# Performance work log

Hardware: AMD Instinct MI355X
Metric: run time of the kernel (lower is better)

The kernel has to match this reference:

```python
import jax, jax.numpy as jnp
import numpy as np

B, L, D, H = 4, 1024, 1024, 16
DK = D // H


def setup_inputs() -> dict:
    key = jax.random.key(0)
    ks = jax.random.split(key, 5)
    s = 1.0 / np.sqrt(D)  # roughly nn.Linear init scale
    return {
        "x": jax.random.normal(ks[0], (B, L, D), dtype=jnp.float32),
        "Wq": jax.random.normal(ks[1], (D, D), dtype=jnp.float32) * s,
        "bq": jnp.zeros((D,), dtype=jnp.float32),
        "Wk": jax.random.normal(ks[2], (D, D), dtype=jnp.float32) * s,
        "bk": jnp.zeros((D,), dtype=jnp.float32),
        "Wv": jax.random.normal(ks[3], (D, D), dtype=jnp.float32) * s,
        "bv": jnp.zeros((D,), dtype=jnp.float32),
        "Wo": jax.random.normal(ks[4], (D, D), dtype=jnp.float32) * s,
        "bo": jnp.zeros((D,), dtype=jnp.float32),
    }


def reference(x, Wq, bq, Wk, bk, Wv, bv, Wo, bo):
    b, l, d = x.shape
    # torch Linear: y = x @ W.T + b
    q = (x @ Wq.T + bq).reshape(b, l, H, DK).transpose(0, 2, 1, 3)  # [B,H,L,DK]
    k = (x @ Wk.T + bk).reshape(b, l, H, DK).transpose(0, 2, 1, 3)
    v = (x @ Wv.T + bv).reshape(b, l, H, DK).transpose(0, 2, 1, 3)
    scores = jnp.einsum("bhqd,bhkd->bhqk", q, k) / jnp.sqrt(jnp.float32(DK))
    attn = jax.nn.softmax(scores, axis=-1)  # dropout p=0 -> identity
    head_out = jnp.einsum("bhqk,bhkd->bhqd", attn, v)  # [B,H,L,DK]
    merged = head_out.transpose(0, 2, 1, 3).reshape(b, l, d)  # [B,L,D]
    out = merged @ Wo.T + bo
    # DeCov loss over head outputs
    U = merged.reshape(b * l, d)
    U = U - U.mean(axis=0, keepdims=True)
    C = (U.T @ U) / jnp.float32(b * l)
    decov = 0.5 * (jnp.sum(C * C) - jnp.sum(jnp.diag(C) ** 2))
    return (out, decov)
```

## Files before the change

### kernel.cpp

```cpp
#include <hip/hip_runtime.h>
#include <cstdint>
#include <cstddef>

typedef short v4s __attribute__((ext_vector_type(4)));
typedef short v8s __attribute__((ext_vector_type(8)));
typedef float v4f __attribute__((ext_vector_type(4)));

__device__ __forceinline__ short f2bf(float f) {
    union { float f; unsigned u; } x; x.f = f;
    unsigned r = (x.u + 0x7FFFu + ((x.u >> 16) & 1u)) >> 16;
    return (short)(unsigned short)r;
}
__device__ __forceinline__ float bf2f(short h) {
    union { unsigned u; float f; } x; x.u = ((unsigned)(unsigned short)h) << 16;
    return x.f;
}

__device__ __forceinline__ void gld16(const void* g, void* l) {
    __builtin_amdgcn_global_load_lds((const __attribute__((address_space(1))) void*)g,
                                     (__attribute__((address_space(3))) void*)l, 16, 0, 0);
}

__global__ __launch_bounds__(256) void cvt_bf16(
    const float* __restrict__ x, const float* __restrict__ wq, const float* __restrict__ wk,
    const float* __restrict__ wv, const float* __restrict__ wo,
    short* __restrict__ xb, short* __restrict__ wqb, short* __restrict__ wkb,
    short* __restrict__ wvb, short* __restrict__ wob, float* __restrict__ colsum,
    float* __restrict__ dtot, int* __restrict__ dcnt)
{
    int bid = blockIdx.x;
    const float* src; short* dst; size_t base;
    if (bid < 4096)      { src = x;  dst = xb;  base = (size_t)bid * 1024; }
    else if (bid < 5120) { src = wq; dst = wqb; base = (size_t)(bid - 4096) * 1024; }
    else if (bid < 6144) { src = wk; dst = wkb; base = (size_t)(bid - 5120) * 1024; }
    else if (bid < 7168) { src = wv; dst = wvb; base = (size_t)(bid - 6144) * 1024; }
    else                 { src = wo; dst = wob; base = (size_t)(bid - 7168) * 1024; }
    size_t idx = base + (size_t)threadIdx.x * 4;
    v4f v = *(const v4f*)(src + idx);
    v4s o;
    o[0] = f2bf(v[0]); o[1] = f2bf(v[1]); o[2] = f2bf(v[2]); o[3] = f2bf(v[3]);
    *(v4s*)(dst + idx) = o;
    if (bid == 0) {
        v4f z = {0.f, 0.f, 0.f, 0.f};
        *(v4f*)(colsum + (size_t)threadIdx.x * 4) = z;
        if (threadIdx.x == 0) { *dtot = 0.f; *dcnt = 0; }
    }
}

__global__ __launch_bounds__(256) void gemm_qkv(
    const short* __restrict__ xb,
    const short* __restrict__ wq, const short* __restrict__ wk, const short* __restrict__ wv,
    const float* __restrict__ bq, const float* __restrict__ bk, const float* __restrict__ bv,
    short* __restrict__ qo, short* __restrict__ ko, short* __restrict__ vto)
{
    __shared__ __align__(16) short At[128 * 32];
    __shared__ __align__(16) short Bt[128 * 32];
    const int K = 1024;
    const int mode = blockIdx.z;
    const short* W = (mode == 0) ? wq : (mode == 1) ? wk : wv;
    const float* bias = (mode == 0) ? bq : (mode == 1) ? bk : bv;
    const int m0 = blockIdx.y * 128, n0 = blockIdx.x * 128;
    const int tid = threadIdx.x, wave = tid >> 6, lane = tid & 63;
    const int quad = lane >> 4, ll = lane & 15;
    const int wr = wave >> 1, wc = wave & 1;
    const v4f zero4 = {0.f, 0.f, 0.f, 0.f};
    v4f acc[4][4];
    for (int i = 0; i < 4; ++i) for (int j = 0; j < 4; ++j) acc[i][j] = zero4;

    for (int k0 = 0; k0 < K; k0 += 32) {
        __syncthreads();
#pragma unroll
        for (int c = 0; c < 2; ++c) {
            int chb = (wave * 2 + c) * 64;
            int ch = chb + lane;
            int row = ch >> 2, col8 = (ch & 3) * 8;
            gld16(xb + (size_t)(m0 + row) * K + k0 + col8, &At[chb * 8]);
            gld16(W  + (size_t)(n0 + row) * K + k0 + col8, &Bt[chb * 8]);
        }
        __syncthreads();
        v8s af[4], bfr[4];
#pragma unroll
        for (int i = 0; i < 4; ++i) af[i]  = *(const v8s*)&At[(wr * 64 + i * 16 + ll) * 32 + quad * 8];
#pragma unroll
        for (int j = 0; j < 4; ++j) bfr[j] = *(const v8s*)&Bt[(wc * 64 + j * 16 + ll) * 32 + quad * 8];
#pragma unroll
        for (int i = 0; i < 4; ++i)
#pragma unroll
            for (int j = 0; j < 4; ++j)
                acc[i][j] = __builtin_amdgcn_mfma_f32_16x16x32_bf16(af[i], bfr[j], acc[i][j], 0, 0, 0);
    }

    const float scale = (mode == 0) ? 0.125f : 1.0f;
#pragma unroll
    for (int j = 0; j < 4; ++j) {
        int n = n0 + wc * 64 + j * 16 + ll;
        float bb = bias[n];
        int hh = n >> 6, dk = n & 63;
#pragma unroll
        for (int i = 0; i < 4; ++i) {
            int mbase = m0 + wr * 64 + i * 16 + quad * 4;
#pragma unroll
            for (int r = 0; r < 4; ++r) {
                int m = mbase + r;
                int b = m >> 10, li = m & 1023;
                short h = f2bf((acc[i][j][r] + bb) * scale);
                if (mode == 0)
                    qo[(((size_t)(b * 16 + hh) * 1024 + li) << 6) + dk] = h;
                else if (mode == 1)
                    ko[(((size_t)(b * 16 + hh) * 1024 + li) << 6) + dk] = h;
                else
                    vto[(((size_t)(b * 16 + hh) * 64 + dk) << 10) + li] = h;
            }
        }
    }
}

__global__ __launch_bounds__(256) void attn_flash(
    const short* __restrict__ qb, const short* __restrict__ kb, const short* __restrict__ vtb,
    float* __restrict__ merged, short* __restrict__ mergedh, float* __restrict__ colsum)
{
    __shared__ __align__(16) short Kt[64 * 64];
    __shared__ __align__(16) short Vt[64 * 64];
    __shared__ __align__(16) short Pt[4 * 32 * 68];
    const int bh = blockIdx.y, qt = blockIdx.x;
    const int tid = threadIdx.x, wave = tid >> 6, lane = tid & 63;
    const int quad = lane >> 4, ll = lane & 15;
    const short* qp = qb  + (size_t)bh * 1024 * 64;
    const short* kp = kb  + (size_t)bh * 1024 * 64;
    const short* vp = vtb + (size_t)bh * 64 * 1024;

    v8s qa[2][2];
#pragma unroll
    for (int mi = 0; mi < 2; ++mi) {
        int qrow = qt * 128 + wave * 32 + mi * 16 + ll;
        qa[mi][0] = *(const v8s*)(qp + (size_t)qrow * 64 + quad * 8);
        qa[mi][1] = *(const v8s*)(qp + (size_t)qrow * 64 + 32 + quad * 8);
    }

    const v4f zero4 = {0.f, 0.f, 0.f, 0.f};
    v4f oacc[2][4];
    for (int mi = 0; mi < 2; ++mi) for (int nt = 0; nt < 4; ++nt) oacc[mi][nt] = zero4;
    float lsum[2][4];
    for (int mi = 0; mi < 2; ++mi) for (int r = 0; r < 4; ++r) lsum[mi][r] = 0.f;
    short* pw = &Pt[wave * 32 * 68];

    for (int jt = 0; jt < 16; ++jt) {
        __syncthreads();
#pragma unroll
        for (int c = 0; c < 2; ++c) {
            int chb = (wave * 2 + c) * 64;
            int ch = chb + lane;
            int row = ch >> 3;
            int gi = ((ch & 7) ^ (row & 7)) * 8;
            gld16(kp + (size_t)(jt * 64 + row) * 64 + gi, &Kt[chb * 8]);
            gld16(vp + (size_t)row * 1024 + jt * 64 + gi, &Vt[chb * 8]);
        }
        __syncthreads();

        v4f sacc[2][4];
#pragma unroll
        for (int nt = 0; nt < 4; ++nt) {
            int n = nt * 16 + ll;
            int g0 = (quad ^ (n & 7)) * 8;
            int g1 = ((4 + quad) ^ (n & 7)) * 8;
            v8s b0 = *(const v8s*)&Kt[n * 64 + g0];
            v8s b1 = *(const v8s*)&Kt[n * 64 + g1];
#pragma unroll
            for (int mi = 0; mi < 2; ++mi) {
                v4f s = zero4;
                s = __builtin_amdgcn_mfma_f32_16x16x32_bf16(qa[mi][0], b0, s, 0, 0, 0);
                s = __builtin_amdgcn_mfma_f32_16x16x32_bf16(qa[mi][1], b1, s, 0, 0, 0);
                sacc[mi][nt] = s;
            }
        }
#pragma unroll
        for (int mi = 0; mi < 2; ++mi)
#pragma unroll
            for (int nt = 0; nt < 4; ++nt)
#pragma unroll
                for (int r = 0; r < 4; ++r) {
                    float e = __expf(sacc[mi][nt][r]);
                    lsum[mi][r] += e;
                    pw[(mi * 16 + quad * 4 + r) * 68 + nt * 16 + ll] = f2bf(e);
                }
        v8s pa[2][2];
#pragma unroll
        for (int mi = 0; mi < 2; ++mi) {
            v4s p00 = *(const v4s*)&pw[(mi * 16 + ll) * 68 + quad * 8];
            v4s p01 = *(const v4s*)&pw[(mi * 16 + ll) * 68 + quad * 8 + 4];
            v4s p10 = *(const v4s*)&pw[(mi * 16 + ll) * 68 + 32 + quad * 8];
            v4s p11 = *(const v4s*)&pw[(mi * 16 + ll) * 68 + 32 + quad * 8 + 4];
            pa[mi][0] = __builtin_shufflevector(p00, p01, 0, 1, 2, 3, 4, 5, 6, 7);
            pa[mi][1] = __builtin_shufflevector(p10, p11, 0, 1, 2, 3, 4, 5, 6, 7);
        }
#pragma unroll
        for (int nt = 0; nt < 4; ++nt) {
            int n = nt * 16 + ll;
            int g0 = (quad ^ (n & 7)) * 8;
            int g1 = ((4 + quad) ^ (n & 7)) * 8;
            v8s v0 = *(const v8s*)&Vt[n * 64 + g0];
            v8s v1 = *(const v8s*)&Vt[n * 64 + g1];
#pragma unroll
            for (int mi = 0; mi < 2; ++mi) {
                oacc[mi][nt] = __builtin_amdgcn_mfma_f32_16x16x32_bf16(pa[mi][0], v0, oacc[mi][nt], 0, 0, 0);
                oacc[mi][nt] = __builtin_amdgcn_mfma_f32_16x16x32_bf16(pa[mi][1], v1, oacc[mi][nt], 0, 0, 0);
            }
        }
    }

    const int b = bh >> 4, h = bh & 15;
    float csum[4] = {0.f, 0.f, 0.f, 0.f};
#pragma unroll
    for (int mi = 0; mi < 2; ++mi) {
        float linv[4];
#pragma unroll
        for (int r = 0; r < 4; ++r) {
            float s = lsum[mi][r];
            s += __shfl_xor(s, 1); s += __shfl_xor(s, 2);
            s += __shfl_xor(s, 4); s += __shfl_xor(s, 8);
            linv[r] = 1.0f / s;
        }
#pragma unroll
        for (int r = 0; r < 4; ++r) {
            int li = qt * 128 + wave * 32 + mi * 16 + quad * 4 + r;
            size_t rowoff = ((size_t)(b * 1024 + li)) * 1024 + h * 64;
#pragma unroll
            for (int nt = 0; nt < 4; ++nt) {
                int d = nt * 16 + ll;
                float v = oacc[mi][nt][r] * linv[r];
                merged[rowoff + d] = v;
                mergedh[rowoff + d] = f2bf(v);
                csum[nt] += v;
            }
        }
    }
#pragma unroll
    for (int nt = 0; nt < 4; ++nt) {
        csum[nt] += __shfl_xor(csum[nt], 16);
        csum[nt] += __shfl_xor(csum[nt], 32);
    }
    if (quad == 0) {
#pragma unroll
        for (int nt = 0; nt < 4; ++nt)
            atomicAdd(&colsum[h * 64 + nt * 16 + ll], csum[nt]);
    }
}

__global__ __launch_bounds__(256) void post_attn(
    const short* __restrict__ A, const short* __restrict__ W, const float* __restrict__ bias,
    float* __restrict__ out,
    const float* __restrict__ merged, const float* __restrict__ colsum,
    short* __restrict__ uth, short* __restrict__ utl)
{
    __shared__ __align__(16) char smem[18432];
    const int bid = blockIdx.x;
    const int tid = threadIdx.x;
    if (bid < 256) {
        short* At = (short*)smem;
        short* Bt = (short*)(smem + 8192);
        const int K = 1024;
        const int n0 = (bid & 7) * 128, m0 = (bid >> 3) * 128;
        const int wave = tid >> 6, lane = tid & 63;
        const int quad = lane >> 4, ll = lane & 15;
        const int wr = wave >> 1, wc = wave & 1;
        const v4f zero4 = {0.f, 0.f, 0.f, 0.f};
        v4f acc[4][4];
        for (int i = 0; i < 4; ++i) for (int j = 0; j < 4; ++j) acc[i][j] = zero4;

        for (int k0 = 0; k0 < K; k0 += 32) {
            __syncthreads();
#pragma unroll
            for (int c = 0; c < 2; ++c) {
                int chb = (wave * 2 + c) * 64;
                int ch = chb + lane;
                int row = ch >> 2, col8 = (ch & 3) * 8;
                gld16(A + (size_t)(m0 + row) * K + k0 + col8, &At[chb * 8]);
                gld16(W + (size_t)(n0 + row) * K + k0 + col8, &Bt[chb * 8]);
            }
            __syncthreads();
            v8s af[4], bfr[4];
#pragma unroll
            for (int i = 0; i < 4; ++i) af[i]  = *(const v8s*)&At[(wr * 64 + i * 16 + ll) * 32 + quad * 8];
#pragma unroll
            for (int j = 0; j < 4; ++j) bfr[j] = *(const v8s*)&Bt[(wc * 64 + j * 16 + ll) * 32 + quad * 8];
#pragma unroll
            for (int i = 0; i < 4; ++i)
#pragma unroll
                for (int j = 0; j < 4; ++j)
                    acc[i][j] = __builtin_amdgcn_mfma_f32_16x16x32_bf16(af[i], bfr[j], acc[i][j], 0, 0, 0);
        }

#pragma unroll
        for (int j = 0; j < 4; ++j) {
            int n = n0 + wc * 64 + j * 16 + ll;
            float bb = bias[n];
#pragma unroll
            for (int i = 0; i < 4; ++i) {
                int mbase = m0 + wr * 64 + i * 16 + quad * 4;
#pragma unroll
                for (int r = 0; r < 4; ++r) {
                    int m = mbase + r;
                    out[(size_t)m * 1024 + n] = acc[i][j][r] + bb;
                }
            }
        }
    } else {
        short (*Hh)[72] = (short(*)[72])smem;
        short (*Hl)[72] = (short(*)[72])(smem + 9216);
        const int cid = bid - 256;
        const int d0 = (cid & 15) * 64, m0 = (cid >> 4) * 64;
        const int r0 = tid >> 4, c4 = (tid & 15) * 4;
        float mu[4];
#pragma unroll
        for (int e = 0; e < 4; ++e) mu[e] = colsum[d0 + c4 + e] * (1.0f / 4096.0f);
        for (int rr = 0; rr < 64; rr += 16) {
            int m = m0 + rr + r0;
            v4f v = *(const v4f*)(merged + (size_t)m * 1024 + d0 + c4);
#pragma unroll
            for (int e = 0; e < 4; ++e) {
                float u = v[e] - mu[e];
                short h = f2bf(u);
                Hh[c4 + e][rr + r0] = h;
                Hl[c4 + e][rr + r0] = f2bf(u - bf2f(h));
            }
        }
        __syncthreads();
        const int d = tid >> 2, mg = (tid & 3) * 16;
        v8s a0, a1, b0, b1;
#pragma unroll
        for (int e = 0; e < 8; ++e) {
            a0[e] = Hh[d][mg + e]; a1[e] = Hh[d][mg + 8 + e];
            b0[e] = Hl[d][mg + e]; b1[e] = Hl[d][mg + 8 + e];
        }
        size_t off = (size_t)(d0 + d) * 4096 + m0 + mg;
        *(v8s*)(uth + off) = a0; *(v8s*)(uth + off + 8) = a1;
        *(v8s*)(utl + off) = b0; *(v8s*)(utl + off + 8) = b1;
    }
}

__global__ __launch_bounds__(256) void gemm_decov(
    const short* __restrict__ uth, const short* __restrict__ utl, float* __restrict__ cpart)
{
    int p = blockIdx.x, I = 0, rem = p;
    while (rem >= 16 - I) { rem -= 16 - I; ++I; }
    const int J = I + rem;
    const int kbase = blockIdx.y * 512;
    __shared__ __align__(16) short Ah[64 * 32], Al[64 * 32], Bh[64 * 32], Bl[64 * 32];
    const int tid = threadIdx.x;
    const int wave = tid >> 6, lane = tid & 63;
    const int quad = lane >> 4, ll = lane & 15;
    const int wr = wave >> 1, wc = wave & 1;
    const v4f zero4 = {0.f, 0.f, 0.f, 0.f};
    v4f acc[2][2];
    for (int i = 0; i < 2; ++i) for (int j = 0; j < 2; ++j) acc[i][j] = zero4;

    for (int kk = 0; kk < 512; kk += 32) {
        int k0 = kbase + kk;
        __syncthreads();
        {
            int ch = wave * 64 + lane;
            int row = ch >> 2, col8 = (ch & 3) * 8;
            gld16(uth + (size_t)(I * 64 + row) * 4096 + k0 + col8, &Ah[wave * 512]);
            gld16(utl + (size_t)(I * 64 + row) * 4096 + k0 + col8, &Al[wave * 512]);
            gld16(uth + (size_t)(J * 64 + row) * 4096 + k0 + col8, &Bh[wave * 512]);
            gld16(utl + (size_t)(J * 64 + row) * 4096 + k0 + col8, &Bl[wave * 512]);
        }
        __syncthreads();
        v8s ah[2], al[2], bh[2], bl[2];
#pragma unroll
        for (int i = 0; i < 2; ++i) {
            int ro = (wr * 32 + i * 16 + ll) * 32 + quad * 8;
            ah[i] = *(const v8s*)&Ah[ro];
            al[i] = *(const v8s*)&Al[ro];
        }
#pragma unroll
        for (int j = 0; j < 2; ++j) {
            int ro = (wc * 32 + j * 16 + ll) * 32 + quad * 8;
            bh[j] = *(const v8s*)&Bh[ro];
            bl[j] = *(const v8s*)&Bl[ro];
        }
#pragma unroll
        for (int i = 0; i < 2; ++i)
#pragma unroll
            for (int j = 0; j < 2; ++j) {
                acc[i][j] = __builtin_amdgcn_mfma_f32_16x16x32_bf16(ah[i], bh[j], acc[i][j], 0, 0, 0);
                acc[i][j] = __builtin_amdgcn_mfma_f32_16x16x32_bf16(ah[i], bl[j], acc[i][j], 0, 0, 0);
                acc[i][j] = __builtin_amdgcn_mfma_f32_16x16x32_bf16(al[i], bh[j], acc[i][j], 0, 0, 0);
            }
    }

    float* dst = cpart + ((size_t)blockIdx.y * 136 + p) * 4096;
#pragma unroll
    for (int i = 0; i < 2; ++i)
#pragma unroll
        for (int j = 0; j < 2; ++j)
#pragma unroll
            for (int r = 0; r < 4; ++r) {
                int gi2 = wr * 32 + i * 16 + quad * 4 + r;
                int gj2 = wc * 32 + j * 16 + ll;
                dst[gi2 * 64 + gj2] = acc[i][j][r];
            }
}

__global__ __launch_bounds__(256) void decov_reduce(
    const float* __restrict__ cpart, float* __restrict__ dtot, int* __restrict__ dcnt,
    float* __restrict__ out)
{
    int p = blockIdx.x, I = 0, rem = p;
    while (rem >= 16 - I) { rem -= 16 - I; ++I; }
    const int J = I + rem;
    const int t = threadIdx.x;
    __shared__ float wsums[4];
    float s = 0.f;
    for (int e = t; e < 4096; e += 256) {
        float c = 0.f;
#pragma unroll
        for (int kc = 0; kc < 8; ++kc) c += cpart[((size_t)kc * 136 + p) * 4096 + e];
        int gi = I * 64 + (e >> 6), gj = J * 64 + (e & 63);
        if (gi != gj) s += c * c;
    }
    if (I < J) s *= 2.f;
    s += __shfl_xor(s, 1); s += __shfl_xor(s, 2); s += __shfl_xor(s, 4);
    s += __shfl_xor(s, 8); s += __shfl_xor(s, 16); s += __shfl_xor(s, 32);
    if ((t & 63) == 0) wsums[t >> 6] = s;
    __syncthreads();
    if (t == 0) {
        float blk = wsums[0] + wsums[1] + wsums[2] + wsums[3];
        float o = atomicAdd(dtot, blk);
        int old = atomicAdd(dcnt, 1 + (int)(o * 0.0f));
        if (old == 135) {
            float tot = atomicAdd(dtot, 0.0f);
            out[4194304] = 0.5f * tot / (4096.0f * 4096.0f);
        }
    }
}

extern "C" void kernel_launch(void* const* d_in, const int* in_sizes, int n_in,
                              void* d_out, int out_size, void* d_ws, size_t ws_size,
                              hipStream_t stream) {
    const float* x  = (const float*)d_in[0];
    const float* Wq = (const float*)d_in[1];
    const float* bq = (const float*)d_in[2];
    const float* Wk = (const float*)d_in[3];
    const float* bk = (const float*)d_in[4];
    const float* Wv = (const float*)d_in[5];
    const float* bv = (const float*)d_in[6];
    const float* Wo = (const float*)d_in[7];
    const float* bo = (const float*)d_in[8];
    float* out = (float*)d_out;
    char* ws = (char*)d_ws;
    const size_t MB = 1ull << 20;
    short* xb      = (short*)(ws);
    short* wqb     = (short*)(ws + 8  * MB);
    short* wkb     = (short*)(ws + 10 * MB);
    short* wvb     = (short*)(ws + 12 * MB);
    short* wob     = (short*)(ws + 14 * MB);
    short* qb      = (short*)(ws + 16 * MB);
    short* kb      = (short*)(ws + 24 * MB);
    short* vtb     = (short*)(ws + 32 * MB);
    float* merged  = (float*)(ws + 40 * MB);
    short* mergedh = (short*)(ws + 56 * MB);
    short* uth     = (short*)(ws + 65 * MB);
    short* utl     = (short*)(ws + 73 * MB);
    float* dtot    = (float*)(ws + 81 * MB);
    int*   dcnt    = (int*)(ws + 81 * MB + 64);
    float* colsum  = (float*)(ws + 81 * MB + 4096);
    float* cpart   = (float*)(ws);

    hipLaunchKernelGGL(cvt_bf16, dim3(8192), dim3(256), 0, stream,
                       x, Wq, Wk, Wv, Wo, xb, wqb, wkb, wvb, wob, colsum, dtot, dcnt);
    hipLaunchKernelGGL(gemm_qkv, dim3(8, 32, 3), dim3(256), 0, stream,
                       xb, wqb, wkb, wvb, bq, bk, bv, qb, kb, vtb);
    hipLaunchKernelGGL(attn_flash, dim3(8, 64), dim3(256), 0, stream,
                       qb, kb, vtb, merged, mergedh, colsum);
    hipLaunchKernelGGL(post_attn, dim3(1280), dim3(256), 0, stream,
                       mergedh, wob, bo, out, merged, colsum, uth, utl);
    hipLaunchKernelGGL(gemm_decov, dim3(136, 8), dim3(256), 0, stream, uth, utl, cpart);
    hipLaunchKernelGGL(decov_reduce, dim3(136), dim3(256), 0, stream, cpart, dtot, dcnt, out);
}
```

Baseline: 237.0 us.

## Enlarge DeCov Gram GEMM tiles to 128x128 with per-wave loading

```diff
diff --git a/kernel.cpp b/kernel.cpp
--- a/kernel.cpp
+++ b/kernel.cpp
@@ -342,63 +342,63 @@
     const short* __restrict__ uth, const short* __restrict__ utl, float* __restrict__ cpart)
 {
     int p = blockIdx.x, I = 0, rem = p;
-    while (rem >= 16 - I) { rem -= 16 - I; ++I; }
+    while (rem >= 8 - I) { rem -= 8 - I; ++I; }
     const int J = I + rem;
-    const int kbase = blockIdx.y * 512;
-    __shared__ __align__(16) short Ah[64 * 32], Al[64 * 32], Bh[64 * 32], Bl[64 * 32];
+    const int kbase = blockIdx.y * 256;
+    __shared__ __align__(16) short Ah[128 * 32], Al[128 * 32], Bh[128 * 32], Bl[128 * 32];
     const int tid = threadIdx.x;
     const int wave = tid >> 6, lane = tid & 63;
     const int quad = lane >> 4, ll = lane & 15;
     const int wr = wave >> 1, wc = wave & 1;
     const v4f zero4 = {0.f, 0.f, 0.f, 0.f};
-    v4f acc[2][2];
-    for (int i = 0; i < 2; ++i) for (int j = 0; j < 2; ++j) acc[i][j] = zero4;
-
-    for (int kk = 0; kk < 512; kk += 32) {
+    v4f acc[4][4];
+    for (int i = 0; i < 4; ++i) for (int j = 0; j < 4; ++j) acc[i][j] = zero4;
+
+    short* sarr = (wave == 0) ? Ah : (wave == 1) ? Al : (wave == 2) ? Bh : Bl;
+    const short* gsrc = (wave & 1) ? utl : uth;
+    const int rbase = ((wave < 2) ? I : J) * 128;
+    const int srow = lane >> 2, scol = (lane & 3) * 8;
+
+    for (int kk = 0; kk < 256; kk += 32) {
         int k0 = kbase + kk;
         __syncthreads();
-        {
-            int ch = wave * 64 + lane;
-            int row = ch >> 2, col8 = (ch & 3) * 8;
-            gld16(uth + (size_t)(I * 64 + row) * 4096 + k0 + col8, &Ah[wave * 512]);
-            gld16(utl + (size_t)(I * 64 + row) * 4096 + k0 + col8, &Al[wave * 512]);
-            gld16(uth + (size_t)(J * 64 + row) * 4096 + k0 + col8, &Bh[wave * 512]);
-            gld16(utl + (size_t)(J * 64 + row) * 4096 + k0 + col8, &Bl[wave * 512]);
-        }
-        __syncthreads();
-        v8s ah[2], al[2], bh[2], bl[2];
-#pragma unroll
-        for (int i = 0; i < 2; ++i) {
-            int ro = (wr * 32 + i * 16 + ll) * 32 + quad * 8;
-            ah[i] = *(const v8s*)&Ah[ro];
-            al[i] = *(const v8s*)&Al[ro];
-        }
-#pragma unroll
-        for (int j = 0; j < 2; ++j) {
-            int ro = (wc * 32 + j * 16 + ll) * 32 + quad * 8;
+#pragma unroll
+        for (int c = 0; c < 8; ++c) {
+            int row = c * 16 + srow;
+            gld16(gsrc + (size_t)(rbase + row) * 4096 + k0 + scol, &sarr[c * 512]);
+        }
+        __syncthreads();
+        v8s bh[4], bl[4];
+#pragma unroll
+        for (int j = 0; j < 4; ++j) {
+            int ro = (wc * 64 + j * 16 + ll) * 32 + quad * 8;
             bh[j] = *(const v8s*)&Bh[ro];
             bl[j] = *(const v8s*)&Bl[ro];
         }
 #pragma unroll
-        for (int i = 0; i < 2; ++i)
-#pragma unroll
-            for (int j = 0; j < 2; ++j) {
-                acc[i][j] = __builtin_amdgcn_mfma_f32_16x16x32_bf16(ah[i], bh[j], acc[i][j], 0, 0, 0);
-                acc[i][j] = __builtin_amdgcn_mfma_f32_16x16x32_bf16(ah[i], bl[j], acc[i][j], 0, 0, 0);
-                acc[i][j] = __builtin_amdgcn_mfma_f32_16x16x32_bf16(al[i], bh[j], acc[i][j], 0, 0, 0);
-            }
-    }
-
-    float* dst = cpart + ((size_t)blockIdx.y * 136 + p) * 4096;
-#pragma unroll
-    for (int i = 0; i < 2; ++i)
-#pragma unroll
-        for (int j = 0; j < 2; ++j)
+        for (int i = 0; i < 4; ++i) {
+            int ro = (wr * 64 + i * 16 + ll) * 32 + quad * 8;
+            v8s ah = *(const v8s*)&Ah[ro];
+            v8s al = *(const v8s*)&Al[ro];
+#pragma unroll
+            for (int j = 0; j < 4; ++j) {
+                acc[i][j] = __builtin_amdgcn_mfma_f32_16x16x32_bf16(ah, bh[j], acc[i][j], 0, 0, 0);
+                acc[i][j] = __builtin_amdgcn_mfma_f32_16x16x32_bf16(ah, bl[j], acc[i][j], 0, 0, 0);
+                acc[i][j] = __builtin_amdgcn_mfma_f32_16x16x32_bf16(al, bh[j], acc[i][j], 0, 0, 0);
+            }
+        }
+    }
+
+    float* dst = cpart + ((size_t)blockIdx.y * 36 + p) * 16384;
+#pragma unroll
+    for (int i = 0; i < 4; ++i)
+#pragma unroll
+        for (int j = 0; j < 4; ++j)
 #pragma unroll
             for (int r = 0; r < 4; ++r) {
-                int gi2 = wr * 32 + i * 16 + quad * 4 + r;
-                int gj2 = wc * 32 + j * 16 + ll;
-                dst[gi2 * 64 + gj2] = acc[i][j][r];
+                int gi2 = wr * 64 + i * 16 + quad * 4 + r;
+                int gj2 = wc * 64 + j * 16 + ll;
+                dst[gi2 * 128 + gj2] = acc[i][j][r];
             }
 }
 
@@ -407,17 +407,25 @@
     float* __restrict__ out)
 {
     int p = blockIdx.x, I = 0, rem = p;
-    while (rem >= 16 - I) { rem -= 16 - I; ++I; }
+    while (rem >= 8 - I) { rem -= 8 - I; ++I; }
     const int J = I + rem;
     const int t = threadIdx.x;
+    const int ebase = blockIdx.y * 4096;
     __shared__ float wsums[4];
     float s = 0.f;
-    for (int e = t; e < 4096; e += 256) {
-        float c = 0.f;
-#pragma unroll
-        for (int kc = 0; kc < 8; ++kc) c += cpart[((size_t)kc * 136 + p) * 4096 + e];
-        int gi = I * 64 + (e >> 6), gj = J * 64 + (e & 63);
-        if (gi != gj) s += c * c;
+#pragma unroll
+    for (int it = 0; it < 4; ++it) {
+        int e4 = ebase + it * 1024 + t * 4;
+        v4f c = {0.f, 0.f, 0.f, 0.f};
+#pragma unroll
+        for (int kc = 0; kc < 16; ++kc)
+            c += *(const v4f*)&cpart[((size_t)kc * 36 + p) * 16384 + e4];
+        int gi = I * 128 + (e4 >> 7), colb = J * 128 + (e4 & 127);
+#pragma unroll
+        for (int k = 0; k < 4; ++k) {
+            float cv = c[k];
+            if (gi != colb + k) s += cv * cv;
+        }
     }
     if (I < J) s *= 2.f;
     s += __shfl_xor(s, 1); s += __shfl_xor(s, 2); s += __shfl_xor(s, 4);
@@ -428,7 +436,7 @@
         float blk = wsums[0] + wsums[1] + wsums[2] + wsums[3];
         float o = atomicAdd(dtot, blk);
         int old = atomicAdd(dcnt, 1 + (int)(o * 0.0f));
-        if (old == 135) {
+        if (old == 143) {
             float tot = atomicAdd(dtot, 0.0f);
             out[4194304] = 0.5f * tot / (4096.0f * 4096.0f);
         }
@@ -475,6 +483,6 @@
                        qb, kb, vtb, merged, mergedh, colsum);
     hipLaunchKernelGGL(post_attn, dim3(1280), dim3(256), 0, stream,
                        mergedh, wob, bo, out, merged, colsum, uth, utl);
-    hipLaunchKernelGGL(gemm_decov, dim3(136, 8), dim3(256), 0, stream, uth, utl, cpart);
-    hipLaunchKernelGGL(decov_reduce, dim3(136), dim3(256), 0, stream, cpart, dtot, dcnt, out);
-}
+    hipLaunchKernelGGL(gemm_decov, dim3(36, 16), dim3(256), 0, stream, uth, utl, cpart);
+    hipLaunchKernelGGL(decov_reduce, dim3(36, 4), dim3(256), 0, stream, cpart, dtot, dcnt, out);
+}
```

Result: no change. 241.0 us (+1.7%).
